# Performance work log

Hardware: AMD Instinct MI355X
Metric: run time of the kernel (lower is better)

Reference implementation:

```python
import jax, jax.numpy as jnp
import numpy as np


def setup_inputs() -> dict:
    key = jax.random.key(0)
    k1, k2 = jax.random.split(key)
    B, H, W, D = 2, 160, 192, 160
    X = jax.random.normal(k1, (B, H, W, D, 2), dtype=jnp.float32)
    deformation = jax.random.normal(k2, (B, H, W, D, 3), dtype=jnp.float32)
    return {"X": X, "deformation": deformation}


def reference(X, deformation):
    # X: (B,H,W,D,2); warp the first channel by the dense deformation field.
    B, H, W, D, _ = X.shape
    Y = X[..., 0:1]                     # (B,H,W,D,1) volume to warp
    N = H * W * D

    # Identity grid, matching tf.meshgrid(x,y,z) 'xy' semantics: shape (H,W,D),
    # x varies along axis1 (width), y along axis0 (height), z along axis2 (depth).
    ys, xs, zs = jnp.meshgrid(
        jnp.arange(H, dtype=jnp.float32),
        jnp.arange(W, dtype=jnp.float32),
        jnp.arange(D, dtype=jnp.float32),
        indexing='ij')

    d = deformation.reshape(B, N, 3)
    x = xs.reshape(-1)[None, :] + d[..., 0]   # (B,N)
    y = ys.reshape(-1)[None, :] + d[..., 1]
    z = zs.reshape(-1)[None, :] + d[..., 2]

    x0 = jnp.floor(x).astype(jnp.int32); x1 = x0 + 1
    y0 = jnp.floor(y).astype(jnp.int32); y1 = y0 + 1
    z0 = jnp.floor(z).astype(jnp.int32); z1 = z0 + 1

    x0 = jnp.clip(x0, 0, W - 1); x1 = jnp.clip(x1, 0, W - 1)
    y0 = jnp.clip(y0, 0, H - 1); y1 = jnp.clip(y1, 0, H - 1)
    z0 = jnp.clip(z0, 0, D - 1); z1 = jnp.clip(z1, 0, D - 1)

    flat = Y.reshape(B, N, 1)           # (B, H*W*D, C=1)

    def gather(yy, xx, zz):
        idx = (yy * (W * D) + xx * D + zz)[..., None]   # (B,N,1)
        return jnp.take_along_axis(flat, idx, axis=1)

    p000 = gather(y0, x0, z0); p001 = gather(y0, x0, z1)
    p010 = gather(y0, x1, z0); p011 = gather(y0, x1, z1)
    p100 = gather(y1, x0, z0); p101 = gather(y1, x0, z1)
    p110 = gather(y1, x1, z0); p111 = gather(y1, x1, z1)

    # Weights use the CLIPPED corner coordinates (faithful to the original).
    x0f = x0.astype(jnp.float32); x1f = x1.astype(jnp.float32)
    y0f = y0.astype(jnp.float32); y1f = y1.astype(jnp.float32)
    z0f = z0.astype(jnp.float32); z1f = z1.astype(jnp.float32)

    w000 = ((y1f - y) * (x1f - x) * (z1f - z))[..., None]
    w001 = ((y1f - y) * (x1f - x) * (z - z0f))[..., None]
    w010 = ((y1f - y) * (x - x0f) * (z1f - z))[..., None]
    w011 = ((y1f - y) * (x - x0f) * (z - z0f))[..., None]
    w100 = ((y - y0f) * (x1f - x) * (z1f - z))[..., None]
    w101 = ((y - y0f) * (x1f - x) * (z - z0f))[..., None]
    w110 = ((y - y0f) * (x - x0f) * (z1f - z))[..., None]
    w111 = ((y - y0f) * (x - x0f) * (z - z0f))[..., None]

    out = (w000 * p000 + w001 * p001 + w010 * p010 + w011 * p011 +
           w100 * p100 + w101 * p101 + w110 * p110 + w111 * p111)
    return out.reshape(B, H, W, D, 1)
```

## Files before the change

kernel.cpp:

```cpp
#include <hip/hip_runtime.h>

#define BB 2
#define HH 160
#define WW 192
#define DD 160
#define NN (HH * WW * DD)
#define TOTAL (BB * NN)

__global__ __launch_bounds__(256)
void SpatialDeformer3D_kernel(const float* __restrict__ X,
                              const float* __restrict__ def,
                              float* __restrict__ out) {
    const int n = blockIdx.x * 256 + threadIdx.x;

    const int b    = n / NN;
    const int rem  = n - b * NN;
    const int h    = rem / (WW * DD);
    const int rem2 = rem - h * (WW * DD);
    const int w    = rem2 / DD;
    const int d    = rem2 - w * DD;

    const float* dp = def + (size_t)n * 3;
    const float x = (float)w + dp[0];
    const float y = (float)h + dp[1];
    const float z = (float)d + dp[2];

    int ix0 = (int)floorf(x);
    int iy0 = (int)floorf(y);
    int iz0 = (int)floorf(z);
    int ix1 = ix0 + 1, iy1 = iy0 + 1, iz1 = iz0 + 1;
    ix0 = min(max(ix0, 0), WW - 1); ix1 = min(max(ix1, 0), WW - 1);
    iy0 = min(max(iy0, 0), HH - 1); iy1 = min(max(iy1, 0), HH - 1);
    iz0 = min(max(iz0, 0), DD - 1); iz1 = min(max(iz1, 0), DD - 1);

    const float x0f = (float)ix0, x1f = (float)ix1;
    const float y0f = (float)iy0, y1f = (float)iy1;
    const float z0f = (float)iz0, z1f = (float)iz1;

    const float wx0 = x1f - x, wx1 = x - x0f;
    const float wy0 = y1f - y, wy1 = y - y0f;
    const float wz0 = z1f - z, wz1 = z - z0f;

    const float* Xb = X + (size_t)b * (2u * (size_t)NN);
    const int ry0 = iy0 * (WW * DD), ry1 = iy1 * (WW * DD);
    const int rx0 = ix0 * DD,        rx1 = ix1 * DD;

    const float p000 = Xb[(size_t)(ry0 + rx0 + iz0) * 2];
    const float p001 = Xb[(size_t)(ry0 + rx0 + iz1) * 2];
    const float p010 = Xb[(size_t)(ry0 + rx1 + iz0) * 2];
    const float p011 = Xb[(size_t)(ry0 + rx1 + iz1) * 2];
    const float p100 = Xb[(size_t)(ry1 + rx0 + iz0) * 2];
    const float p101 = Xb[(size_t)(ry1 + rx0 + iz1) * 2];
    const float p110 = Xb[(size_t)(ry1 + rx1 + iz0) * 2];
    const float p111 = Xb[(size_t)(ry1 + rx1 + iz1) * 2];

    const float r =
        wy0 * (wx0 * (wz0 * p000 + wz1 * p001) + wx1 * (wz0 * p010 + wz1 * p011)) +
        wy1 * (wx0 * (wz0 * p100 + wz1 * p101) + wx1 * (wz0 * p110 + wz1 * p111));

    out[n] = r;
}

extern "C" void kernel_launch(void* const* d_in, const int* in_sizes, int n_in,
                              void* d_out, int out_size, void* d_ws, size_t ws_size,
                              hipStream_t stream) {
    const float* X   = (const float*)d_in[0];
    const float* def = (const float*)d_in[1];
    float* out = (float*)d_out;

    const int blocks = TOTAL / 256;
    SpatialDeformer3D_kernel<<<blocks, 256, 0, stream>>>(X, def, out);
}
```

Baseline: 304.5 us.

## Compact channel 0 into workspace and gather z-pairs with 8-byte loads

Adds a pre-pass that copies channel 0 of X into a dense workspace buffer. The gather kernel then reads each (y,x) corner pair along z with one unaligned 8-byte load, so it issues four loads per voxel instead of eight strided scalar loads. Clamped z edges are handled by picking lo/hi from the pair. This costs an extra kernel launch plus a full read of X and a write of the workspace. If the workspace is too small it falls back to the original direct kernel.

Result: faster. 279.2 us (-8.3%).

```diff
diff --git a/kernel.cpp b/kernel.cpp
--- a/kernel.cpp
+++ b/kernel.cpp
@@ -7,10 +7,82 @@
 #define NN (HH * WW * DD)
 #define TOTAL (BB * NN)
 
+struct __attribute__((packed, aligned(4))) f2u { float lo, hi; };
+
 __global__ __launch_bounds__(256)
-void SpatialDeformer3D_kernel(const float* __restrict__ X,
+void compact_ch0_kernel(const float4* __restrict__ X4, float4* __restrict__ C4) {
+    const int i = blockIdx.x * 256 + threadIdx.x;
+    const float4 a = X4[2 * i];
+    const float4 b = X4[2 * i + 1];
+    C4[i] = make_float4(a.x, a.z, b.x, b.z);
+}
+
+__global__ __launch_bounds__(256)
+void SpatialDeformer3D_kernel(const float* __restrict__ C,
                               const float* __restrict__ def,
                               float* __restrict__ out) {
+    const int n = blockIdx.x * 256 + threadIdx.x;
+
+    const int b    = n / NN;
+    const int rem  = n - b * NN;
+    const int h    = rem / (WW * DD);
+    const int rem2 = rem - h * (WW * DD);
+    const int w    = rem2 / DD;
+    const int d    = rem2 - w * DD;
+
+    const float* dp = def + (size_t)n * 3;
+    const float x = (float)w + dp[0];
+    const float y = (float)h + dp[1];
+    const float z = (float)d + dp[2];
+
+    int ix0 = (int)floorf(x);
+    int iy0 = (int)floorf(y);
+    int iz0 = (int)floorf(z);
+    int ix1 = ix0 + 1, iy1 = iy0 + 1;
+    ix0 = min(max(ix0, 0), WW - 1); ix1 = min(max(ix1, 0), WW - 1);
+    iy0 = min(max(iy0, 0), HH - 1); iy1 = min(max(iy1, 0), HH - 1);
+    const int czlo = min(max(iz0, 0), DD - 1);
+    const int czhi = min(max(iz0 + 1, 0), DD - 1);
+    const int zb   = min(max(iz0, 0), DD - 2);
+
+    const float wx0 = (float)ix1 - x, wx1 = x - (float)ix0;
+    const float wy0 = (float)iy1 - y, wy1 = y - (float)iy0;
+    const float wz0 = (float)czhi - z, wz1 = z - (float)czlo;
+
+    const bool lo_is_v0 = (czlo == zb);
+    const bool hi_is_v1 = (czhi == zb + 1);
+
+    const float* Cb = C + (size_t)b * NN;
+    const int r00 = iy0 * (WW * DD) + ix0 * DD + zb;
+    const int r01 = iy0 * (WW * DD) + ix1 * DD + zb;
+    const int r10 = iy1 * (WW * DD) + ix0 * DD + zb;
+    const int r11 = iy1 * (WW * DD) + ix1 * DD + zb;
+
+    const f2u v00 = *(const f2u*)(Cb + r00);
+    const f2u v01 = *(const f2u*)(Cb + r01);
+    const f2u v10 = *(const f2u*)(Cb + r10);
+    const f2u v11 = *(const f2u*)(Cb + r11);
+
+    const float p000 = lo_is_v0 ? v00.lo : v00.hi;
+    const float p001 = hi_is_v1 ? v00.hi : v00.lo;
+    const float p010 = lo_is_v0 ? v01.lo : v01.hi;
+    const float p011 = hi_is_v1 ? v01.hi : v01.lo;
+    const float p100 = lo_is_v0 ? v10.lo : v10.hi;
+    const float p101 = hi_is_v1 ? v10.hi : v10.lo;
+    const float p110 = lo_is_v0 ? v11.lo : v11.hi;
+    const float p111 = hi_is_v1 ? v11.hi : v11.lo;
+
+    const float r =
+        wy0 * (wx0 * (wz0 * p000 + wz1 * p001) + wx1 * (wz0 * p010 + wz1 * p011)) +
+        wy1 * (wx0 * (wz0 * p100 + wz1 * p101) + wx1 * (wz0 * p110 + wz1 * p111));
+
+    out[n] = r;
+}
+
+__global__ __launch_bounds__(256)
+void SpatialDeformer3D_direct_kernel(const float* __restrict__ X,
+                                     const float* __restrict__ def,
+                                     float* __restrict__ out) {
     const int n = blockIdx.x * 256 + threadIdx.x;
 
     const int b    = n / NN;
@@ -33,13 +105,9 @@
     iy0 = min(max(iy0, 0), HH - 1); iy1 = min(max(iy1, 0), HH - 1);
     iz0 = min(max(iz0, 0), DD - 1); iz1 = min(max(iz1, 0), DD - 1);
 
-    const float x0f = (float)ix0, x1f = (float)ix1;
-    const float y0f = (float)iy0, y1f = (float)iy1;
-    const float z0f = (float)iz0, z1f = (float)iz1;
-
-    const float wx0 = x1f - x, wx1 = x - x0f;
-    const float wy0 = y1f - y, wy1 = y - y0f;
-    const float wz0 = z1f - z, wz1 = z - z0f;
+    const float wx0 = (float)ix1 - x, wx1 = x - (float)ix0;
+    const float wy0 = (float)iy1 - y, wy1 = y - (float)iy0;
+    const float wz0 = (float)iz1 - z, wz1 = z - (float)iz0;
 
     const float* Xb = X + (size_t)b * (2u * (size_t)NN);
     const int ry0 = iy0 * (WW * DD), ry1 = iy1 * (WW * DD);
@@ -68,6 +136,13 @@
     const float* def = (const float*)d_in[1];
     float* out = (float*)d_out;
 
-    const int blocks = TOTAL / 256;
-    SpatialDeformer3D_kernel<<<blocks, 256, 0, stream>>>(X, def, out);
+    const size_t need = (size_t)TOTAL * sizeof(float);
+    if (ws_size >= need) {
+        float* C = (float*)d_ws;
+        compact_ch0_kernel<<<TOTAL / 4 / 256, 256, 0, stream>>>(
+            (const float4*)X, (float4*)C);
+        SpatialDeformer3D_kernel<<<TOTAL / 256, 256, 0, stream>>>(C, def, out);
+    } else {
+        SpatialDeformer3D_direct_kernel<<<TOTAL / 256, 256, 0, stream>>>(X, def, out);
+    }
 }
```

## Process four voxels per thread with vector loads and paired z-corner gathers

Applied to the files above, without the earlier changes.

Each thread now handles four consecutive depth voxels. It reads the deformation with three float4 loads, writes the output with one float4 store, and fetches each pair of z-adjacent corners with a single 16-byte load from the interleaved 2-channel volume instead of two scalar loads. The aim is to cut the number of memory instructions and to improve coalescing on the deformation reads and output writes. In exchange, each thread carries more registers, the grid is four times smaller, the 16-byte gather loads are only 8-byte aligned, and clamped z edges need extra select logic.

New measurement: 341.5 us. +12.2%, slower.

```diff
diff --git a/kernel.cpp b/kernel.cpp
--- a/kernel.cpp
+++ b/kernel.cpp
@@ -7,58 +7,82 @@
 #define NN (HH * WW * DD)
 #define TOTAL (BB * NN)
 
+struct __attribute__((packed, aligned(8))) f4u { float x, y, z, w; };
+
 __global__ __launch_bounds__(256)
 void SpatialDeformer3D_kernel(const float* __restrict__ X,
                               const float* __restrict__ def,
                               float* __restrict__ out) {
-    const int n = blockIdx.x * 256 + threadIdx.x;
+    const int t  = blockIdx.x * 256 + threadIdx.x;
+    const int n0 = t * 4;
 
-    const int b    = n / NN;
-    const int rem  = n - b * NN;
+    const int b    = n0 / NN;
+    const int rem  = n0 - b * NN;
     const int h    = rem / (WW * DD);
     const int rem2 = rem - h * (WW * DD);
     const int w    = rem2 / DD;
-    const int d    = rem2 - w * DD;
+    const int d0   = rem2 - w * DD;
 
-    const float* dp = def + (size_t)n * 3;
-    const float x = (float)w + dp[0];
-    const float y = (float)h + dp[1];
-    const float z = (float)d + dp[2];
+    const float4* dp = (const float4*)(def + (size_t)n0 * 3);
+    const float4 D0 = dp[0];
+    const float4 D1 = dp[1];
+    const float4 D2 = dp[2];
 
-    int ix0 = (int)floorf(x);
-    int iy0 = (int)floorf(y);
-    int iz0 = (int)floorf(z);
-    int ix1 = ix0 + 1, iy1 = iy0 + 1, iz1 = iz0 + 1;
-    ix0 = min(max(ix0, 0), WW - 1); ix1 = min(max(ix1, 0), WW - 1);
-    iy0 = min(max(iy0, 0), HH - 1); iy1 = min(max(iy1, 0), HH - 1);
-    iz0 = min(max(iz0, 0), DD - 1); iz1 = min(max(iz1, 0), DD - 1);
-
-    const float x0f = (float)ix0, x1f = (float)ix1;
-    const float y0f = (float)iy0, y1f = (float)iy1;
-    const float z0f = (float)iz0, z1f = (float)iz1;
-
-    const float wx0 = x1f - x, wx1 = x - x0f;
-    const float wy0 = y1f - y, wy1 = y - y0f;
-    const float wz0 = z1f - z, wz1 = z - z0f;
+    const float dxs[4] = {D0.x, D0.w, D1.z, D2.y};
+    const float dys[4] = {D0.y, D1.x, D1.w, D2.z};
+    const float dzs[4] = {D0.z, D1.y, D2.x, D2.w};
 
     const float* Xb = X + (size_t)b * (2u * (size_t)NN);
-    const int ry0 = iy0 * (WW * DD), ry1 = iy1 * (WW * DD);
-    const int rx0 = ix0 * DD,        rx1 = ix1 * DD;
+    float res[4];
 
-    const float p000 = Xb[(size_t)(ry0 + rx0 + iz0) * 2];
-    const float p001 = Xb[(size_t)(ry0 + rx0 + iz1) * 2];
-    const float p010 = Xb[(size_t)(ry0 + rx1 + iz0) * 2];
-    const float p011 = Xb[(size_t)(ry0 + rx1 + iz1) * 2];
-    const float p100 = Xb[(size_t)(ry1 + rx0 + iz0) * 2];
-    const float p101 = Xb[(size_t)(ry1 + rx0 + iz1) * 2];
-    const float p110 = Xb[(size_t)(ry1 + rx1 + iz0) * 2];
-    const float p111 = Xb[(size_t)(ry1 + rx1 + iz1) * 2];
+#pragma unroll
+    for (int k = 0; k < 4; ++k) {
+        const float x = (float)w + dxs[k];
+        const float y = (float)h + dys[k];
+        const float z = (float)(d0 + k) + dzs[k];
 
-    const float r =
-        wy0 * (wx0 * (wz0 * p000 + wz1 * p001) + wx1 * (wz0 * p010 + wz1 * p011)) +
-        wy1 * (wx0 * (wz0 * p100 + wz1 * p101) + wx1 * (wz0 * p110 + wz1 * p111));
+        int ix0 = (int)floorf(x);
+        int iy0 = (int)floorf(y);
+        int iz0 = (int)floorf(z);
+        int ix1 = ix0 + 1, iy1 = iy0 + 1;
+        ix0 = min(max(ix0, 0), WW - 1); ix1 = min(max(ix1, 0), WW - 1);
+        iy0 = min(max(iy0, 0), HH - 1); iy1 = min(max(iy1, 0), HH - 1);
+        const int czlo = min(max(iz0, 0), DD - 1);
+        const int czhi = min(max(iz0 + 1, 0), DD - 1);
+        const int zb   = min(max(iz0, 0), DD - 2);
 
-    out[n] = r;
+        const float wx0 = (float)ix1 - x, wx1 = x - (float)ix0;
+        const float wy0 = (float)iy1 - y, wy1 = y - (float)iy0;
+        const float wz0 = (float)czhi - z, wz1 = z - (float)czlo;
+
+        const bool lo_is_v0 = (czlo == zb);
+        const bool hi_is_v1 = (czhi == zb + 1);
+
+        const int r00 = iy0 * (WW * DD) + ix0 * DD + zb;
+        const int r01 = iy0 * (WW * DD) + ix1 * DD + zb;
+        const int r10 = iy1 * (WW * DD) + ix0 * DD + zb;
+        const int r11 = iy1 * (WW * DD) + ix1 * DD + zb;
+
+        const f4u v00 = *(const f4u*)(Xb + (size_t)r00 * 2);
+        const f4u v01 = *(const f4u*)(Xb + (size_t)r01 * 2);
+        const f4u v10 = *(const f4u*)(Xb + (size_t)r10 * 2);
+        const f4u v11 = *(const f4u*)(Xb + (size_t)r11 * 2);
+
+        const float p000 = lo_is_v0 ? v00.x : v00.z;
+        const float p001 = hi_is_v1 ? v00.z : v00.x;
+        const float p010 = lo_is_v0 ? v01.x : v01.z;
+        const float p011 = hi_is_v1 ? v01.z : v01.x;
+        const float p100 = lo_is_v0 ? v10.x : v10.z;
+        const float p101 = hi_is_v1 ? v10.z : v10.x;
+        const float p110 = lo_is_v0 ? v11.x : v11.z;
+        const float p111 = hi_is_v1 ? v11.z : v11.x;
+
+        res[k] =
+            wy0 * (wx0 * (wz0 * p000 + wz1 * p001) + wx1 * (wz0 * p010 + wz1 * p011)) +
+            wy1 * (wx0 * (wz0 * p100 + wz1 * p101) + wx1 * (wz0 * p110 + wz1 * p111));
+    }
+
+    *(float4*)(out + n0) = make_float4(res[0], res[1], res[2], res[3]);
 }
 
 extern "C" void kernel_launch(void* const* d_in, const int* in_sizes, int n_in,
@@ -68,6 +92,6 @@
     const float* def = (const float*)d_in[1];
     float* out = (float*)d_out;
 
-    const int blocks = TOTAL / 256;
+    const int blocks = (TOTAL / 4) / 256;
     SpatialDeformer3D_kernel<<<blocks, 256, 0, stream>>>(X, def, out);
 }
```

## Stage halo tile of source volume in LDS as bf16 for trilinear gathers

Applied to the files above, without the earlier changes.

Each block processes a 16x16x16 output tile. It first loads a 25^3 halo window of the source channel into shared memory, stored as bf16. Corner samples that fall inside the window are read from LDS, and the rest fall back to global gathers. The aim is to replace scattered global gathers with LDS reads. This costs redundant halo loads, reduced precision for in-window samples, and a block-wide sync before compute.

Result: slower. 325.7 us (+6.9%).

```diff
diff --git a/kernel.cpp b/kernel.cpp
--- a/kernel.cpp
+++ b/kernel.cpp
@@ -4,61 +4,133 @@
 #define HH 160
 #define WW 192
 #define DD 160
+#define WD (WW * DD)
 #define NN (HH * WW * DD)
-#define TOTAL (BB * NN)
+
+#define TS 16
+#define M  4
+#define SY 25
+#define SX 25
+#define SZ 25
+#define ZP 26
+#define YSTR (SX * ZP)
+#define SN (SY * SX * SZ)
+#define LDS_ELEMS (SY * YSTR)
+
+#define NTH (HH / TS)
+#define NTW (WW / TS)
+#define NTD (DD / TS)
+#define NBLK (BB * NTH * NTW * NTD)
+
+__device__ inline unsigned short f2bf(float f) {
+    unsigned u = __builtin_bit_cast(unsigned, f);
+    u += 0x7FFFu + ((u >> 16) & 1u);
+    return (unsigned short)(u >> 16);
+}
+__device__ inline float bf2f(unsigned short s) {
+    return __builtin_bit_cast(float, (unsigned)s << 16);
+}
+
+struct __attribute__((packed, aligned(4))) f3u { float x, y, z; };
 
 __global__ __launch_bounds__(256)
 void SpatialDeformer3D_kernel(const float* __restrict__ X,
                               const float* __restrict__ def,
                               float* __restrict__ out) {
-    const int n = blockIdx.x * 256 + threadIdx.x;
+    __shared__ unsigned short tile[LDS_ELEMS];
 
-    const int b    = n / NN;
-    const int rem  = n - b * NN;
-    const int h    = rem / (WW * DD);
-    const int rem2 = rem - h * (WW * DD);
-    const int w    = rem2 / DD;
-    const int d    = rem2 - w * DD;
+    int id = blockIdx.x;
+    const int b  = id / (NTH * NTW * NTD);
+    int r        = id - b * (NTH * NTW * NTD);
+    const int th = r / (NTW * NTD);
+    r           -= th * (NTW * NTD);
+    const int tw = r / NTD;
+    const int td = r - tw * NTD;
 
-    const float* dp = def + (size_t)n * 3;
-    const float x = (float)w + dp[0];
-    const float y = (float)h + dp[1];
-    const float z = (float)d + dp[2];
-
-    int ix0 = (int)floorf(x);
-    int iy0 = (int)floorf(y);
-    int iz0 = (int)floorf(z);
-    int ix1 = ix0 + 1, iy1 = iy0 + 1, iz1 = iz0 + 1;
-    ix0 = min(max(ix0, 0), WW - 1); ix1 = min(max(ix1, 0), WW - 1);
-    iy0 = min(max(iy0, 0), HH - 1); iy1 = min(max(iy1, 0), HH - 1);
-    iz0 = min(max(iz0, 0), DD - 1); iz1 = min(max(iz1, 0), DD - 1);
-
-    const float x0f = (float)ix0, x1f = (float)ix1;
-    const float y0f = (float)iy0, y1f = (float)iy1;
-    const float z0f = (float)iz0, z1f = (float)iz1;
-
-    const float wx0 = x1f - x, wx1 = x - x0f;
-    const float wy0 = y1f - y, wy1 = y - y0f;
-    const float wz0 = z1f - z, wz1 = z - z0f;
+    const int h0 = th * TS, w0 = tw * TS, z0 = td * TS;
+    const int ylo = h0 - M, xlo = w0 - M, zlo = z0 - M;
+    const int yhi = h0 + TS + M, xhi = w0 + TS + M, zhi = z0 + TS + M;
 
     const float* Xb = X + (size_t)b * (2u * (size_t)NN);
-    const int ry0 = iy0 * (WW * DD), ry1 = iy1 * (WW * DD);
-    const int rx0 = ix0 * DD,        rx1 = ix1 * DD;
 
-    const float p000 = Xb[(size_t)(ry0 + rx0 + iz0) * 2];
-    const float p001 = Xb[(size_t)(ry0 + rx0 + iz1) * 2];
-    const float p010 = Xb[(size_t)(ry0 + rx1 + iz0) * 2];
-    const float p011 = Xb[(size_t)(ry0 + rx1 + iz1) * 2];
-    const float p100 = Xb[(size_t)(ry1 + rx0 + iz0) * 2];
-    const float p101 = Xb[(size_t)(ry1 + rx0 + iz1) * 2];
-    const float p110 = Xb[(size_t)(ry1 + rx1 + iz0) * 2];
-    const float p111 = Xb[(size_t)(ry1 + rx1 + iz1) * 2];
+    for (int e = threadIdx.x; e < SN; e += 256) {
+        const int ly = e / (SX * SZ);
+        const int r2 = e - ly * (SX * SZ);
+        const int lx = r2 / SZ;
+        const int lz = r2 - lx * SZ;
+        const int gy = min(max(ylo + ly, 0), HH - 1);
+        const int gx = min(max(xlo + lx, 0), WW - 1);
+        const int gz = min(max(zlo + lz, 0), DD - 1);
+        const float v = Xb[(size_t)(gy * WD + gx * DD + gz) * 2];
+        tile[ly * YSTR + lx * ZP + lz] = f2bf(v);
+    }
+    __syncthreads();
 
-    const float r =
-        wy0 * (wx0 * (wz0 * p000 + wz1 * p001) + wx1 * (wz0 * p010 + wz1 * p011)) +
-        wy1 * (wx0 * (wz0 * p100 + wz1 * p101) + wx1 * (wz0 * p110 + wz1 * p111));
+    const int lxT = threadIdx.x >> 4;
+    const int lzT = threadIdx.x & 15;
+    const int w   = w0 + lxT;
+    const int dpos = z0 + lzT;
 
-    out[n] = r;
+#pragma unroll 2
+    for (int ly = 0; ly < TS; ++ly) {
+        const int h = h0 + ly;
+        const int n = (b * HH + h) * WD + w * DD + dpos;
+
+        const f3u dv = *(const f3u*)(def + (size_t)n * 3);
+        const float x = (float)w + dv.x;
+        const float y = (float)h + dv.y;
+        const float z = (float)dpos + dv.z;
+
+        int ix0 = (int)floorf(x);
+        int iy0 = (int)floorf(y);
+        int iz0 = (int)floorf(z);
+        int ix1 = ix0 + 1, iy1 = iy0 + 1, iz1 = iz0 + 1;
+        ix0 = min(max(ix0, 0), WW - 1); ix1 = min(max(ix1, 0), WW - 1);
+        iy0 = min(max(iy0, 0), HH - 1); iy1 = min(max(iy1, 0), HH - 1);
+        iz0 = min(max(iz0, 0), DD - 1); iz1 = min(max(iz1, 0), DD - 1);
+
+        const float wx0 = (float)ix1 - x, wx1 = x - (float)ix0;
+        const float wy0 = (float)iy1 - y, wy1 = y - (float)iy0;
+        const float wz0 = (float)iz1 - z, wz1 = z - (float)iz0;
+
+        const bool inwin = (iy0 >= ylo) & (iy1 <= yhi) &
+                           (ix0 >= xlo) & (ix1 <= xhi) &
+                           (iz0 >= zlo) & (iz1 <= zhi);
+
+        float p000, p001, p010, p011, p100, p101, p110, p111;
+        if (inwin) {
+            const int ay0 = (iy0 - ylo) * YSTR, ay1 = (iy1 - ylo) * YSTR;
+            const int ax0 = (ix0 - xlo) * ZP,   ax1 = (ix1 - xlo) * ZP;
+            const int az0 = iz0 - zlo,          az1 = iz1 - zlo;
+            p000 = bf2f(tile[ay0 + ax0 + az0]);
+            p001 = bf2f(tile[ay0 + ax0 + az1]);
+            p010 = bf2f(tile[ay0 + ax1 + az0]);
+            p011 = bf2f(tile[ay0 + ax1 + az1]);
+            p100 = bf2f(tile[ay1 + ax0 + az0]);
+            p101 = bf2f(tile[ay1 + ax0 + az1]);
+            p110 = bf2f(tile[ay1 + ax1 + az0]);
+            p111 = bf2f(tile[ay1 + ax1 + az1]);
+        } else {
+            const int r00 = iy0 * WD + ix0 * DD;
+            const int r01 = iy0 * WD + ix1 * DD;
+            const int r10 = iy1 * WD + ix0 * DD;
+            const int r11 = iy1 * WD + ix1 * DD;
+            p000 = Xb[(size_t)(r00 + iz0) * 2];
+            p001 = Xb[(size_t)(r00 + iz1) * 2];
+            p010 = Xb[(size_t)(r01 + iz0) * 2];
+            p011 = Xb[(size_t)(r01 + iz1) * 2];
+            p100 = Xb[(size_t)(r10 + iz0) * 2];
+            p101 = Xb[(size_t)(r10 + iz1) * 2];
+            p110 = Xb[(size_t)(r11 + iz0) * 2];
+            p111 = Xb[(size_t)(r11 + iz1) * 2];
+        }
+
+        const float res =
+            wy0 * (wx0 * (wz0 * p000 + wz1 * p001) + wx1 * (wz0 * p010 + wz1 * p011)) +
+            wy1 * (wx0 * (wz0 * p100 + wz1 * p101) + wx1 * (wz0 * p110 + wz1 * p111));
+
+        out[n] = res;
+    }
 }
 
 extern "C" void kernel_launch(void* const* d_in, const int* in_sizes, int n_in,
@@ -68,6 +140,5 @@
     const float* def = (const float*)d_in[1];
     float* out = (float*)d_out;
 
-    const int blocks = TOTAL / 256;
-    SpatialDeformer3D_kernel<<<blocks, 256, 0, stream>>>(X, def, out);
+    SpatialDeformer3D_kernel<<<NBLK, 256, 0, stream>>>(X, def, out);
 }
```
